# Optimization experiments

Hardware: AMD Instinct MI355X
Metric: run time of the kernel (lower is better)

## Reference

```python
import jax, jax.numpy as jnp
import numpy as np

NUM_COLORS = 30
B, C, H, W = 8, 3, 512, 512


def setup_inputs() -> dict:
    key = jax.random.key(0)
    k1, k2 = jax.random.split(key)
    adv_patch = jax.random.uniform(k1, (B, C, H, W), dtype=jnp.float32)
    printability = jax.random.uniform(k2, (NUM_COLORS, C), dtype=jnp.float32)
    return {"adv_patch": adv_patch, "printability": printability}


def reference(adv_patch, printability):
    # printability_array buffer: (num_colors, 1, 3, 1, 1)
    pa = printability[:, None, :, None, None]
    # color_dist: (num_colors, B, 3, H, W) broadcast difference
    color_dist = adv_patch[None] - pa + 1e-6
    color_dist = jnp.sum(color_dist ** 2, axis=2) + 1e-6  # (num_colors, B, H, W)
    color_dist = jnp.sqrt(color_dist)
    color_dist_prod = jnp.min(color_dist, axis=0)  # (B, H, W) min over colors
    nps_score = jnp.sum(color_dist_prod)
    return nps_score / adv_patch.size
```

## Files before the change

kernel.cpp:

```cpp
#include <hip/hip_runtime.h>


#define NPS_HW   (512 * 512)
#define NPS_B    8
#define NPS_NPIX (NPS_B * NPS_HW)
#define NPS_NCOL 30
#define NPS_NBLK 2048
#define NPS_INV_TOTAL (1.0f / 6291456.0f)

__global__ __launch_bounds__(256) void nps_partial_kernel(
    const float* __restrict__ patch,
    const float* __restrict__ prt,
    float* __restrict__ partial)
{
    __shared__ float4 sp[NPS_NCOL];
    __shared__ float wave_part[4];

    const int t = threadIdx.x;
    if (t < NPS_NCOL) {
        float p0 = prt[t * 3 + 0];
        float p1 = prt[t * 3 + 1];
        float p2 = prt[t * 3 + 2];
        sp[t] = make_float4(p0, p1, p2, p0 * p0 + p1 * p1 + p2 * p2);
    }
    __syncthreads();

    const int gid = blockIdx.x * 256 + t;
    const int pix = gid << 2;
    const int b   = pix >> 18;
    const int hw  = pix & (NPS_HW - 1);

    const float* base = patch + (size_t)b * 3 * NPS_HW + hw;
    const float4 x0 = *(const float4*)(base);
    const float4 x1 = *(const float4*)(base + NPS_HW);
    const float4 x2 = *(const float4*)(base + 2 * NPS_HW);

    float y0[4] = { x0.x + 1e-6f, x0.y + 1e-6f, x0.z + 1e-6f, x0.w + 1e-6f };
    float y1[4] = { x1.x + 1e-6f, x1.y + 1e-6f, x1.z + 1e-6f, x1.w + 1e-6f };
    float y2[4] = { x2.x + 1e-6f, x2.y + 1e-6f, x2.z + 1e-6f, x2.w + 1e-6f };

    float hh[4];
#pragma unroll
    for (int i = 0; i < 4; ++i) {
        hh[i] = fmaf(y0[i], y0[i], fmaf(y1[i], y1[i], y2[i] * y2[i])) + 1e-6f;
    }

    float m[4] = { 1e30f, 1e30f, 1e30f, 1e30f };

#pragma unroll 6
    for (int k = 0; k < NPS_NCOL; ++k) {
        const float4 p = sp[k];
#pragma unroll
        for (int i = 0; i < 4; ++i) {
            float dot = fmaf(y0[i], p.x, fmaf(y1[i], p.y, y2[i] * p.z));
            float u   = fmaf(-2.0f, dot, p.w);
            m[i] = fminf(m[i], u);
        }
    }

    float s = 0.0f;
#pragma unroll
    for (int i = 0; i < 4; ++i) {
        s += sqrtf(fmaxf(hh[i] + m[i], 0.0f));
    }

#pragma unroll
    for (int off = 32; off > 0; off >>= 1) {
        s += __shfl_down(s, off);
    }
    const int lane = t & 63;
    const int w    = t >> 6;
    if (lane == 0) wave_part[w] = s;
    __syncthreads();
    if (t == 0) {
        partial[blockIdx.x] = (wave_part[0] + wave_part[1]) + (wave_part[2] + wave_part[3]);
    }
}

__global__ __launch_bounds__(256) void nps_final_kernel(
    const float* __restrict__ partial,
    float* __restrict__ out)
{
    __shared__ float wave_part[4];
    const int t = threadIdx.x;

    float s = 0.0f;
#pragma unroll
    for (int i = 0; i < NPS_NBLK / 256; ++i) {
        s += partial[i * 256 + t];
    }
#pragma unroll
    for (int off = 32; off > 0; off >>= 1) {
        s += __shfl_down(s, off);
    }
    const int lane = t & 63;
    const int w    = t >> 6;
    if (lane == 0) wave_part[w] = s;
    __syncthreads();
    if (t == 0) {
        out[0] = ((wave_part[0] + wave_part[1]) + (wave_part[2] + wave_part[3])) * NPS_INV_TOTAL;
    }
}

extern "C" void kernel_launch(void* const* d_in, const int* in_sizes, int n_in,
                              void* d_out, int out_size, void* d_ws, size_t ws_size,
                              hipStream_t stream) {
    const float* patch = (const float*)d_in[0];
    const float* prt   = (const float*)d_in[1];
    float* out     = (float*)d_out;
    float* partial = (float*)d_ws;

    nps_partial_kernel<<<NPS_NBLK, 256, 0, stream>>>(patch, prt, partial);
    nps_final_kernel<<<1, 256, 0, stream>>>(partial, out);
}
```

Before: 74.17 us.

## Fuse partial and final reduction via cooperative grid sync, 8 pixels per thread

Replaces the two-kernel reduction with one cooperative kernel that writes per-block partials, runs a grid-wide sync, and has block 0 do the final sum. The separate final-kernel launch is dropped, and the old two-kernel path stays as a fallback if the cooperative launch fails. Each thread now handles 8 pixels instead of 4, with half the blocks. The -2 factor is folded into the palette, which removes one FMA per color-pixel pair. Grid sync has a cost of its own, and the 1024 blocks must all be co-resident on the device.

```diff
diff --git a/kernel.cpp b/kernel.cpp
--- a/kernel.cpp
+++ b/kernel.cpp
@@ -1,19 +1,71 @@
 #include <hip/hip_runtime.h>
+#include <hip/hip_cooperative_groups.h>
+
+namespace cg = cooperative_groups;
 
 
 #define NPS_HW   (512 * 512)
 #define NPS_B    8
 #define NPS_NPIX (NPS_B * NPS_HW)
 #define NPS_NCOL 30
-#define NPS_NBLK 2048
+#define NPS_NBLK 1024
 #define NPS_INV_TOTAL (1.0f / 6291456.0f)
 
-__global__ __launch_bounds__(256) void nps_partial_kernel(
+__device__ __forceinline__ float nps_thread_sum(
+    const float* __restrict__ patch, const float4* sq, int gid)
+{
+    const int pix = gid << 3;
+    const int b   = pix >> 18;
+    const int hw  = pix & (NPS_HW - 1);
+
+    const float* base = patch + (size_t)b * 3 * NPS_HW + hw;
+    const float4 xa0 = *(const float4*)(base);
+    const float4 xb0 = *(const float4*)(base + 4);
+    const float4 xa1 = *(const float4*)(base + NPS_HW);
+    const float4 xb1 = *(const float4*)(base + NPS_HW + 4);
+    const float4 xa2 = *(const float4*)(base + 2 * NPS_HW);
+    const float4 xb2 = *(const float4*)(base + 2 * NPS_HW + 4);
+
+    float y0[8] = { xa0.x + 1e-6f, xa0.y + 1e-6f, xa0.z + 1e-6f, xa0.w + 1e-6f,
+                    xb0.x + 1e-6f, xb0.y + 1e-6f, xb0.z + 1e-6f, xb0.w + 1e-6f };
+    float y1[8] = { xa1.x + 1e-6f, xa1.y + 1e-6f, xa1.z + 1e-6f, xa1.w + 1e-6f,
+                    xb1.x + 1e-6f, xb1.y + 1e-6f, xb1.z + 1e-6f, xb1.w + 1e-6f };
+    float y2[8] = { xa2.x + 1e-6f, xa2.y + 1e-6f, xa2.z + 1e-6f, xa2.w + 1e-6f,
+                    xb2.x + 1e-6f, xb2.y + 1e-6f, xb2.z + 1e-6f, xb2.w + 1e-6f };
+
+    float hh[8];
+#pragma unroll
+    for (int i = 0; i < 8; ++i) {
+        hh[i] = fmaf(y0[i], y0[i], fmaf(y1[i], y1[i], fmaf(y2[i], y2[i], 1e-6f)));
+    }
+
+    float m[8] = { 1e30f, 1e30f, 1e30f, 1e30f, 1e30f, 1e30f, 1e30f, 1e30f };
+
+#pragma unroll 6
+    for (int k = 0; k < NPS_NCOL; ++k) {
+        const float4 q = sq[k];
+#pragma unroll
+        for (int i = 0; i < 8; ++i) {
+            float u = fmaf(y0[i], q.x, fmaf(y1[i], q.y, fmaf(y2[i], q.z, q.w)));
+            m[i] = fminf(m[i], u);
+        }
+    }
+
+    float s = 0.0f;
+#pragma unroll
+    for (int i = 0; i < 8; ++i) {
+        s += sqrtf(fmaxf(hh[i] + m[i], 0.0f));
+    }
+    return s;
+}
+
+__global__ __launch_bounds__(256, 4) void nps_fused_kernel(
     const float* __restrict__ patch,
     const float* __restrict__ prt,
-    float* __restrict__ partial)
+    float* __restrict__ partial,
+    float* __restrict__ out)
 {
-    __shared__ float4 sp[NPS_NCOL];
+    __shared__ float4 sq[NPS_NCOL];
     __shared__ float wave_part[4];
 
     const int t = threadIdx.x;
@@ -21,48 +73,67 @@
         float p0 = prt[t * 3 + 0];
         float p1 = prt[t * 3 + 1];
         float p2 = prt[t * 3 + 2];
-        sp[t] = make_float4(p0, p1, p2, p0 * p0 + p1 * p1 + p2 * p2);
+        sq[t] = make_float4(-2.0f * p0, -2.0f * p1, -2.0f * p2,
+                            fmaf(p0, p0, fmaf(p1, p1, p2 * p2)));
     }
     __syncthreads();
 
-    const int gid = blockIdx.x * 256 + t;
-    const int pix = gid << 2;
-    const int b   = pix >> 18;
-    const int hw  = pix & (NPS_HW - 1);
+    float s = nps_thread_sum(patch, sq, blockIdx.x * 256 + t);
 
-    const float* base = patch + (size_t)b * 3 * NPS_HW + hw;
-    const float4 x0 = *(const float4*)(base);
-    const float4 x1 = *(const float4*)(base + NPS_HW);
-    const float4 x2 = *(const float4*)(base + 2 * NPS_HW);
-
-    float y0[4] = { x0.x + 1e-6f, x0.y + 1e-6f, x0.z + 1e-6f, x0.w + 1e-6f };
-    float y1[4] = { x1.x + 1e-6f, x1.y + 1e-6f, x1.z + 1e-6f, x1.w + 1e-6f };
-    float y2[4] = { x2.x + 1e-6f, x2.y + 1e-6f, x2.z + 1e-6f, x2.w + 1e-6f };
-
-    float hh[4];
 #pragma unroll
-    for (int i = 0; i < 4; ++i) {
-        hh[i] = fmaf(y0[i], y0[i], fmaf(y1[i], y1[i], y2[i] * y2[i])) + 1e-6f;
+    for (int off = 32; off > 0; off >>= 1) {
+        s += __shfl_down(s, off);
+    }
+    const int lane = t & 63;
+    const int w    = t >> 6;
+    if (lane == 0) wave_part[w] = s;
+    __syncthreads();
+    if (t == 0) {
+        float bs = (wave_part[0] + wave_part[1]) + (wave_part[2] + wave_part[3]);
+        __hip_atomic_store(&partial[blockIdx.x], bs,
+                           __ATOMIC_RELEASE, __HIP_MEMORY_SCOPE_AGENT);
     }
 
-    float m[4] = { 1e30f, 1e30f, 1e30f, 1e30f };
+    cg::this_grid().sync();
 
-#pragma unroll 6
-    for (int k = 0; k < NPS_NCOL; ++k) {
-        const float4 p = sp[k];
+    if (blockIdx.x == 0) {
+        float v =
+            (__hip_atomic_load(&partial[t],       __ATOMIC_ACQUIRE, __HIP_MEMORY_SCOPE_AGENT) +
+             __hip_atomic_load(&partial[t + 256], __ATOMIC_ACQUIRE, __HIP_MEMORY_SCOPE_AGENT)) +
+            (__hip_atomic_load(&partial[t + 512], __ATOMIC_ACQUIRE, __HIP_MEMORY_SCOPE_AGENT) +
+             __hip_atomic_load(&partial[t + 768], __ATOMIC_ACQUIRE, __HIP_MEMORY_SCOPE_AGENT));
 #pragma unroll
-        for (int i = 0; i < 4; ++i) {
-            float dot = fmaf(y0[i], p.x, fmaf(y1[i], p.y, y2[i] * p.z));
-            float u   = fmaf(-2.0f, dot, p.w);
-            m[i] = fminf(m[i], u);
+        for (int off = 32; off > 0; off >>= 1) {
+            v += __shfl_down(v, off);
+        }
+        if (lane == 0) wave_part[w] = v;
+        __syncthreads();
+        if (t == 0) {
+            out[0] = ((wave_part[0] + wave_part[1]) + (wave_part[2] + wave_part[3])) * NPS_INV_TOTAL;
         }
     }
+}
 
-    float s = 0.0f;
-#pragma unroll
-    for (int i = 0; i < 4; ++i) {
-        s += sqrtf(fmaxf(hh[i] + m[i], 0.0f));
+
+__global__ __launch_bounds__(256) void nps_partial_kernel(
+    const float* __restrict__ patch,
+    const float* __restrict__ prt,
+    float* __restrict__ partial)
+{
+    __shared__ float4 sq[NPS_NCOL];
+    __shared__ float wave_part[4];
+
+    const int t = threadIdx.x;
+    if (t < NPS_NCOL) {
+        float p0 = prt[t * 3 + 0];
+        float p1 = prt[t * 3 + 1];
+        float p2 = prt[t * 3 + 2];
+        sq[t] = make_float4(-2.0f * p0, -2.0f * p1, -2.0f * p2,
+                            fmaf(p0, p0, fmaf(p1, p1, p2 * p2)));
     }
+    __syncthreads();
+
+    float s = nps_thread_sum(patch, sq, blockIdx.x * 256 + t);
 
 #pragma unroll
     for (int off = 32; off > 0; off >>= 1) {
@@ -84,18 +155,14 @@
     __shared__ float wave_part[4];
     const int t = threadIdx.x;
 
-    float s = 0.0f;
-#pragma unroll
-    for (int i = 0; i < NPS_NBLK / 256; ++i) {
-        s += partial[i * 256 + t];
-    }
+    float v = (partial[t] + partial[t + 256]) + (partial[t + 512] + partial[t + 768]);
 #pragma unroll
     for (int off = 32; off > 0; off >>= 1) {
-        s += __shfl_down(s, off);
+        v += __shfl_down(v, off);
     }
     const int lane = t & 63;
     const int w    = t >> 6;
-    if (lane == 0) wave_part[w] = s;
+    if (lane == 0) wave_part[w] = v;
     __syncthreads();
     if (t == 0) {
         out[0] = ((wave_part[0] + wave_part[1]) + (wave_part[2] + wave_part[3])) * NPS_INV_TOTAL;
@@ -110,6 +177,11 @@
     float* out     = (float*)d_out;
     float* partial = (float*)d_ws;
 
-    nps_partial_kernel<<<NPS_NBLK, 256, 0, stream>>>(patch, prt, partial);
-    nps_final_kernel<<<1, 256, 0, stream>>>(partial, out);
+    void* args[] = { (void*)&patch, (void*)&prt, (void*)&partial, (void*)&out };
+    hipError_t e = hipLaunchCooperativeKernel((const void*)nps_fused_kernel,
+                                              dim3(NPS_NBLK), dim3(256), args, 0, stream);
+    if (e != hipSuccess) {
+        nps_partial_kernel<<<NPS_NBLK, 256, 0, stream>>>(patch, prt, partial);
+        nps_final_kernel<<<1, 256, 0, stream>>>(partial, out);
+    }
 }
```

Result: slower. 199.3 us (+168.8%).

## Fuse final reduction via last-block atomic counter and process 16 pixels per thread

Applied to the files above, without the earlier changes.

Merges the two-kernel reduction into a single kernel: each block publishes its partial sum, bumps an atomic counter, and the last block to arrive reduces all partials and writes the output. Each thread now handles 16 pixels instead of 4, with 512 blocks. The -2 scale is folded into the palette so each distance costs three FMAs. A hipMemsetAsync resets the counter, which replaces the second kernel launch with a memset node. The higher register pressure from 16 pixels per thread may cut occupancy.

```diff
diff --git a/kernel.cpp b/kernel.cpp
--- a/kernel.cpp
+++ b/kernel.cpp
@@ -5,62 +5,80 @@
 #define NPS_B    8
 #define NPS_NPIX (NPS_B * NPS_HW)
 #define NPS_NCOL 30
-#define NPS_NBLK 2048
+#define NPS_NBLK 512
+#define NPS_PPT  16
 #define NPS_INV_TOTAL (1.0f / 6291456.0f)
+#define NPS_CTR_OFF 1024
 
-__global__ __launch_bounds__(256) void nps_partial_kernel(
+__global__ __launch_bounds__(256, 2) void nps_onepass_kernel(
     const float* __restrict__ patch,
     const float* __restrict__ prt,
-    float* __restrict__ partial)
+    float* __restrict__ partial,
+    float* __restrict__ out)
 {
-    __shared__ float4 sp[NPS_NCOL];
+    __shared__ float4 sq[NPS_NCOL];
     __shared__ float wave_part[4];
+    __shared__ int   last_flag;
 
     const int t = threadIdx.x;
     if (t < NPS_NCOL) {
         float p0 = prt[t * 3 + 0];
         float p1 = prt[t * 3 + 1];
         float p2 = prt[t * 3 + 2];
-        sp[t] = make_float4(p0, p1, p2, p0 * p0 + p1 * p1 + p2 * p2);
+        sq[t] = make_float4(-2.0f * p0, -2.0f * p1, -2.0f * p2,
+                            fmaf(p0, p0, fmaf(p1, p1, p2 * p2)));
     }
     __syncthreads();
 
     const int gid = blockIdx.x * 256 + t;
-    const int pix = gid << 2;
+    const int pix = gid << 4;
     const int b   = pix >> 18;
     const int hw  = pix & (NPS_HW - 1);
 
     const float* base = patch + (size_t)b * 3 * NPS_HW + hw;
-    const float4 x0 = *(const float4*)(base);
-    const float4 x1 = *(const float4*)(base + NPS_HW);
-    const float4 x2 = *(const float4*)(base + 2 * NPS_HW);
 
-    float y0[4] = { x0.x + 1e-6f, x0.y + 1e-6f, x0.z + 1e-6f, x0.w + 1e-6f };
-    float y1[4] = { x1.x + 1e-6f, x1.y + 1e-6f, x1.z + 1e-6f, x1.w + 1e-6f };
-    float y2[4] = { x2.x + 1e-6f, x2.y + 1e-6f, x2.z + 1e-6f, x2.w + 1e-6f };
+    float4 x0[4], x1[4], x2[4];
+#pragma unroll
+    for (int j = 0; j < 4; ++j) x0[j] = *(const float4*)(base + j * 4);
+#pragma unroll
+    for (int j = 0; j < 4; ++j) x1[j] = *(const float4*)(base + NPS_HW + j * 4);
+#pragma unroll
+    for (int j = 0; j < 4; ++j) x2[j] = *(const float4*)(base + 2 * NPS_HW + j * 4);
 
-    float hh[4];
+    float y0[NPS_PPT], y1[NPS_PPT], y2[NPS_PPT], hh[NPS_PPT], m[NPS_PPT];
 #pragma unroll
-    for (int i = 0; i < 4; ++i) {
-        hh[i] = fmaf(y0[i], y0[i], fmaf(y1[i], y1[i], y2[i] * y2[i])) + 1e-6f;
+    for (int j = 0; j < 4; ++j) {
+        const float* f0 = (const float*)&x0[j];
+        const float* f1 = (const float*)&x1[j];
+        const float* f2 = (const float*)&x2[j];
+#pragma unroll
+        for (int e = 0; e < 4; ++e) {
+            const int i = j * 4 + e;
+            y0[i] = f0[e] + 1e-6f;
+            y1[i] = f1[e] + 1e-6f;
+            y2[i] = f2[e] + 1e-6f;
+        }
     }
 
-    float m[4] = { 1e30f, 1e30f, 1e30f, 1e30f };
+#pragma unroll
+    for (int i = 0; i < NPS_PPT; ++i) {
+        hh[i] = fmaf(y0[i], y0[i], fmaf(y1[i], y1[i], fmaf(y2[i], y2[i], 1e-6f)));
+        m[i]  = 1e30f;
+    }
 
-#pragma unroll 6
+#pragma unroll 3
     for (int k = 0; k < NPS_NCOL; ++k) {
-        const float4 p = sp[k];
+        const float4 q = sq[k];
 #pragma unroll
-        for (int i = 0; i < 4; ++i) {
-            float dot = fmaf(y0[i], p.x, fmaf(y1[i], p.y, y2[i] * p.z));
-            float u   = fmaf(-2.0f, dot, p.w);
+        for (int i = 0; i < NPS_PPT; ++i) {
+            float u = fmaf(y0[i], q.x, fmaf(y1[i], q.y, fmaf(y2[i], q.z, q.w)));
             m[i] = fminf(m[i], u);
         }
     }
 
     float s = 0.0f;
 #pragma unroll
-    for (int i = 0; i < 4; ++i) {
+    for (int i = 0; i < NPS_PPT; ++i) {
         s += sqrtf(fmaxf(hh[i] + m[i], 0.0f));
     }
 
@@ -72,33 +90,30 @@
     const int w    = t >> 6;
     if (lane == 0) wave_part[w] = s;
     __syncthreads();
+
     if (t == 0) {
-        partial[blockIdx.x] = (wave_part[0] + wave_part[1]) + (wave_part[2] + wave_part[3]);
+        float bs = (wave_part[0] + wave_part[1]) + (wave_part[2] + wave_part[3]);
+        __hip_atomic_store(&partial[blockIdx.x], bs,
+                           __ATOMIC_RELEASE, __HIP_MEMORY_SCOPE_AGENT);
+        unsigned old = __hip_atomic_fetch_add((unsigned*)&partial[NPS_CTR_OFF], 1u,
+                                              __ATOMIC_ACQ_REL, __HIP_MEMORY_SCOPE_AGENT);
+        last_flag = (old == (unsigned)(NPS_NBLK - 1)) ? 1 : 0;
     }
-}
+    __syncthreads();
 
-__global__ __launch_bounds__(256) void nps_final_kernel(
-    const float* __restrict__ partial,
-    float* __restrict__ out)
-{
-    __shared__ float wave_part[4];
-    const int t = threadIdx.x;
-
-    float s = 0.0f;
+    if (last_flag) {
+        float v = __hip_atomic_load(&partial[t],       __ATOMIC_ACQUIRE, __HIP_MEMORY_SCOPE_AGENT)
+                + __hip_atomic_load(&partial[t + 256], __ATOMIC_ACQUIRE, __HIP_MEMORY_SCOPE_AGENT);
 #pragma unroll
-    for (int i = 0; i < NPS_NBLK / 256; ++i) {
-        s += partial[i * 256 + t];
-    }
-#pragma unroll
-    for (int off = 32; off > 0; off >>= 1) {
-        s += __shfl_down(s, off);
-    }
-    const int lane = t & 63;
-    const int w    = t >> 6;
-    if (lane == 0) wave_part[w] = s;
-    __syncthreads();
-    if (t == 0) {
-        out[0] = ((wave_part[0] + wave_part[1]) + (wave_part[2] + wave_part[3])) * NPS_INV_TOTAL;
+        for (int off = 32; off > 0; off >>= 1) {
+            v += __shfl_down(v, off);
+        }
+        if (lane == 0) wave_part[w] = v;
+        __syncthreads();
+        if (t == 0) {
+            float r = ((wave_part[0] + wave_part[1]) + (wave_part[2] + wave_part[3])) * NPS_INV_TOTAL;
+            __hip_atomic_store(out, r, __ATOMIC_RELEASE, __HIP_MEMORY_SCOPE_AGENT);
+        }
     }
 }
 
@@ -107,9 +122,10 @@
                               hipStream_t stream) {
     const float* patch = (const float*)d_in[0];
     const float* prt   = (const float*)d_in[1];
-    float* out     = (float*)d_out;
-    float* partial = (float*)d_ws;
+    float* out = (float*)d_out;
+    float* ws  = (float*)d_ws;
 
-    nps_partial_kernel<<<NPS_NBLK, 256, 0, stream>>>(patch, prt, partial);
-    nps_final_kernel<<<1, 256, 0, stream>>>(partial, out);
+    hipMemsetAsync((void*)(ws + NPS_CTR_OFF), 0, sizeof(unsigned), stream);
+
+    nps_onepass_kernel<<<NPS_NBLK, 256, 0, stream>>>(patch, prt, ws, out);
 }
```

New measurement: 87.72 us. 1.18x slower.

## Fold -2 scale into palette, process 8 pixels per thread with nontemporal loads

Applied to the files above, without the earlier changes.

Each palette entry now stores its components pre-scaled by -2 plus its squared norm, so the inner distance test becomes a single chain of three FMAs instead of a dot product followed by a separate FMA. Each thread handles 8 pixels instead of 4 through two vector loads per channel, using nontemporal load builtins, which halves the block count to 1024. The final reduction is rewritten for the smaller partial array. More pixels per thread raise register use but give more independent work per palette load from shared memory.

```diff
diff --git a/kernel.cpp b/kernel.cpp
--- a/kernel.cpp
+++ b/kernel.cpp
@@ -2,18 +2,18 @@
 
 
 #define NPS_HW   (512 * 512)
-#define NPS_B    8
-#define NPS_NPIX (NPS_B * NPS_HW)
 #define NPS_NCOL 30
-#define NPS_NBLK 2048
+#define NPS_NBLK 1024
 #define NPS_INV_TOTAL (1.0f / 6291456.0f)
+
+typedef float vf4 __attribute__((ext_vector_type(4)));
 
 __global__ __launch_bounds__(256) void nps_partial_kernel(
     const float* __restrict__ patch,
     const float* __restrict__ prt,
     float* __restrict__ partial)
 {
-    __shared__ float4 sp[NPS_NCOL];
+    __shared__ float4 sq[NPS_NCOL];
     __shared__ float wave_part[4];
 
     const int t = threadIdx.x;
@@ -21,46 +21,55 @@
         float p0 = prt[t * 3 + 0];
         float p1 = prt[t * 3 + 1];
         float p2 = prt[t * 3 + 2];
-        sp[t] = make_float4(p0, p1, p2, p0 * p0 + p1 * p1 + p2 * p2);
+        sq[t] = make_float4(-2.0f * p0, -2.0f * p1, -2.0f * p2,
+                            fmaf(p0, p0, fmaf(p1, p1, p2 * p2)));
     }
     __syncthreads();
 
     const int gid = blockIdx.x * 256 + t;
-    const int pix = gid << 2;
+    const int pix = gid << 3;
     const int b   = pix >> 18;
     const int hw  = pix & (NPS_HW - 1);
 
-    const float* base = patch + (size_t)b * 3 * NPS_HW + hw;
-    const float4 x0 = *(const float4*)(base);
-    const float4 x1 = *(const float4*)(base + NPS_HW);
-    const float4 x2 = *(const float4*)(base + 2 * NPS_HW);
+    const vf4* p0v = (const vf4*)(patch + (size_t)b * 3 * NPS_HW + hw);
+    const vf4* p1v = (const vf4*)((const float*)p0v + NPS_HW);
+    const vf4* p2v = (const vf4*)((const float*)p0v + 2 * NPS_HW);
 
-    float y0[4] = { x0.x + 1e-6f, x0.y + 1e-6f, x0.z + 1e-6f, x0.w + 1e-6f };
-    float y1[4] = { x1.x + 1e-6f, x1.y + 1e-6f, x1.z + 1e-6f, x1.w + 1e-6f };
-    float y2[4] = { x2.x + 1e-6f, x2.y + 1e-6f, x2.z + 1e-6f, x2.w + 1e-6f };
+    const vf4 xa0 = __builtin_nontemporal_load(p0v);
+    const vf4 xb0 = __builtin_nontemporal_load(p0v + 1);
+    const vf4 xa1 = __builtin_nontemporal_load(p1v);
+    const vf4 xb1 = __builtin_nontemporal_load(p1v + 1);
+    const vf4 xa2 = __builtin_nontemporal_load(p2v);
+    const vf4 xb2 = __builtin_nontemporal_load(p2v + 1);
 
-    float hh[4];
+    float y0[8] = { xa0.x + 1e-6f, xa0.y + 1e-6f, xa0.z + 1e-6f, xa0.w + 1e-6f,
+                    xb0.x + 1e-6f, xb0.y + 1e-6f, xb0.z + 1e-6f, xb0.w + 1e-6f };
+    float y1[8] = { xa1.x + 1e-6f, xa1.y + 1e-6f, xa1.z + 1e-6f, xa1.w + 1e-6f,
+                    xb1.x + 1e-6f, xb1.y + 1e-6f, xb1.z + 1e-6f, xb1.w + 1e-6f };
+    float y2[8] = { xa2.x + 1e-6f, xa2.y + 1e-6f, xa2.z + 1e-6f, xa2.w + 1e-6f,
+                    xb2.x + 1e-6f, xb2.y + 1e-6f, xb2.z + 1e-6f, xb2.w + 1e-6f };
+
+    float hh[8];
 #pragma unroll
-    for (int i = 0; i < 4; ++i) {
-        hh[i] = fmaf(y0[i], y0[i], fmaf(y1[i], y1[i], y2[i] * y2[i])) + 1e-6f;
+    for (int i = 0; i < 8; ++i) {
+        hh[i] = fmaf(y0[i], y0[i], fmaf(y1[i], y1[i], fmaf(y2[i], y2[i], 1e-6f)));
     }
 
-    float m[4] = { 1e30f, 1e30f, 1e30f, 1e30f };
+    float m[8] = { 1e30f, 1e30f, 1e30f, 1e30f, 1e30f, 1e30f, 1e30f, 1e30f };
 
 #pragma unroll 6
     for (int k = 0; k < NPS_NCOL; ++k) {
-        const float4 p = sp[k];
+        const float4 q = sq[k];
 #pragma unroll
-        for (int i = 0; i < 4; ++i) {
-            float dot = fmaf(y0[i], p.x, fmaf(y1[i], p.y, y2[i] * p.z));
-            float u   = fmaf(-2.0f, dot, p.w);
+        for (int i = 0; i < 8; ++i) {
+            float u = fmaf(y0[i], q.x, fmaf(y1[i], q.y, fmaf(y2[i], q.z, q.w)));
             m[i] = fminf(m[i], u);
         }
     }
 
     float s = 0.0f;
 #pragma unroll
-    for (int i = 0; i < 4; ++i) {
+    for (int i = 0; i < 8; ++i) {
         s += sqrtf(fmaxf(hh[i] + m[i], 0.0f));
     }
 
@@ -84,18 +93,14 @@
     __shared__ float wave_part[4];
     const int t = threadIdx.x;
 
-    float s = 0.0f;
-#pragma unroll
-    for (int i = 0; i < NPS_NBLK / 256; ++i) {
-        s += partial[i * 256 + t];
-    }
+    float v = (partial[t] + partial[t + 256]) + (partial[t + 512] + partial[t + 768]);
 #pragma unroll
     for (int off = 32; off > 0; off >>= 1) {
-        s += __shfl_down(s, off);
+        v += __shfl_down(v, off);
     }
     const int lane = t & 63;
     const int w    = t >> 6;
-    if (lane == 0) wave_part[w] = s;
+    if (lane == 0) wave_part[w] = v;
     __syncthreads();
     if (t == 0) {
         out[0] = ((wave_part[0] + wave_part[1]) + (wave_part[2] + wave_part[3])) * NPS_INV_TOTAL;
```

Measured after the change: 75.42 us. No clear change (+1.7%).
